# Kernel tuning notes

Hardware: AMD Instinct MI355X
Metric: run time of the kernel (lower is better)

The kernel has to match this reference:

```python
import jax, jax.numpy as jnp
import numpy as np
import math

REG = 0.1      # entropic regularization (self.reg)
TEMP = 0.1     # self.temperature from kwargs
ITERS = 20     # self.iters
EPS = 1e-5     # torch LayerNorm eps
ALPHA_BOTH = -100.0


def _layernorm(t, g, b):
    mu = jnp.mean(t, axis=-1, keepdims=True)
    var = jnp.mean((t - mu) ** 2, axis=-1, keepdims=True)
    return (t - mu) / jnp.sqrt(var + EPS) * g + b


def setup_inputs() -> dict:
    key = jax.random.key(0)
    k1, k2, k3 = jax.random.split(key, 3)
    B, M, N, H = 2048, 36, 36, 768
    x = jax.random.normal(k1, (B, M, H), jnp.float32)
    y = jax.random.normal(k2, (B, N, H), jnp.float32)
    # dustbin scorer params: LayerNorm(H) -> Linear(H, 1)
    ln_g = jnp.ones((H,), jnp.float32)
    ln_b = jnp.zeros((H,), jnp.float32)
    w = jax.random.normal(k3, (H, 1), jnp.float32) * (1.0 / math.sqrt(H))
    b_lin = jnp.zeros((1,), jnp.float32)
    return {"x": x, "y": y, "ln_g": ln_g, "ln_b": ln_b, "w": w, "b_lin": b_lin}


def reference(x, y, ln_g, ln_b, w, b_lin):
    B, M, H = x.shape
    N = y.shape[1]
    # CosineScorer(temperature=1).score(x, y, get_diag=False)
    xn = x / jnp.linalg.norm(x, axis=-1, keepdims=True)
    yn = y / jnp.linalg.norm(y, axis=-1, keepdims=True)
    scores = jnp.einsum('bmh,bnh->bmn', xn, yn)            # (B, M, N)
    # tanh-clipped learned dustbin scores
    ax = jnp.tanh(_layernorm(x, ln_g, ln_b) @ w + b_lin)   # (B, M, 1)
    ay = jnp.tanh(_layernorm(y, ln_g, ln_b) @ w + b_lin)   # (B, N, 1)
    # augmented score matrix with dustbin row/col
    alpha_both = jnp.full((B, 1, 1), ALPHA_BOTH, scores.dtype)
    top = jnp.concatenate([scores, ax], axis=2)                       # (B, M, N+1)
    bot = jnp.concatenate([jnp.swapaxes(ay, 1, 2), alpha_both], axis=2)  # (B, 1, N+1)
    couplings = jnp.concatenate([top, bot], axis=1) / REG             # (B, M+1, N+1)
    # SuperGlue-style marginals: dustbins absorb the complementary mass
    norm_c = -math.log(M + N)
    log_mu = jnp.concatenate([jnp.full((M,), norm_c),
                              jnp.array([math.log(N) + norm_c])]).astype(scores.dtype)
    log_nu = jnp.concatenate([jnp.full((N,), norm_c),
                              jnp.array([math.log(M) + norm_c])]).astype(scores.dtype)

    def body(carry, _):
        u, v = carry
        u = log_mu[None, :] - jax.nn.logsumexp(couplings + v[:, None, :], axis=2)
        v = log_nu[None, :] - jax.nn.logsumexp(couplings + u[:, :, None], axis=1)
        return (u, v), None

    u0 = jnp.zeros((B, M + 1), scores.dtype)
    v0 = jnp.zeros((B, N + 1), scores.dtype)
    (u, v), _ = jax.lax.scan(body, (u0, v0), None, length=ITERS)
    Z = couplings + u[:, :, None] + v[:, None, :] - norm_c            # log matching, (B, M+1, N+1)
    # scalar alignment score per batch element: <P, S> / temperature
    total = jnp.sum(jnp.exp(Z[:, :-1, :-1]) * scores, axis=(1, 2)) / TEMP
    return Z, total
```

## Files before the change

### kernel.cpp

```cpp
#include <hip/hip_runtime.h>
#include <stdint.h>
#include <stddef.h>


typedef float  f4  __attribute__((ext_vector_type(4)));
typedef short  s8v __attribute__((ext_vector_type(8)));
typedef unsigned int u2v __attribute__((ext_vector_type(2)));

#define HD   768
#define MR   36
#define KC   128
#define NCH  6
#define AS   136
#define CS   44
#define LOG2E 1.4426950408889634f
#define LN2   0.6931471805599453f
#define L272  6.169925001442312f
#define KC2   (10.0f*LOG2E)
#define NEGB  (-1.0e30f)

__device__ __forceinline__ uint32_t pkbf2(float a, float b) {
    uint32_t ua = __float_as_uint(a), ub = __float_as_uint(b);
    ua += 0x7FFFu + ((ua >> 16) & 1u);
    ub += 0x7FFFu + ((ub >> 16) & 1u);
    return (ua >> 16) | (ub & 0xFFFF0000u);
}

__global__ __launch_bounds__(256, 3) void sinkhorn_kernel(
    const float* __restrict__ X, const float* __restrict__ Y,
    const float* __restrict__ LG, const float* __restrict__ LB,
    const float* __restrict__ W,  const float* __restrict__ BL,
    float* __restrict__ OUT, int NB)
{
    __shared__ __align__(16) uint16_t Al[48 * AS];
    __shared__ __align__(16) uint16_t Bt[48 * AS];
    __shared__ __align__(16) float C2 [37 * CS];
    __shared__ __align__(16) float C2T[37 * CS];
    __shared__ __align__(16) float u_l[40];
    __shared__ __align__(16) float v_l[40];
    __shared__ float stx[MR * 3], sty[MR * 3];
    __shared__ float rnx[MR], rny[MR];
    __shared__ float s_gw, s_bw, red[4];

    const int t  = threadIdx.x;
    const int b  = blockIdx.x;
    const int wv = t >> 6, ln = t & 63;
    const int c4 = t & 31, gg = t >> 5;

    if (t < 40) { u_l[t] = 0.0f; v_l[t] = 0.0f; }
    if (t < 37) {
        C2 [t * CS + 37] = NEGB; C2 [t * CS + 38] = NEGB; C2 [t * CS + 39] = NEGB;
        C2T[t * CS + 37] = NEGB; C2T[t * CS + 38] = NEGB; C2T[t * CS + 39] = NEGB;
    }
    if (wv == 3) {
        float a = 0.0f, c = 0.0f;
        for (int q = 0; q < 12; ++q) {
            int h = ln + 64 * q;
            float wval = W[h];
            a += LG[h] * wval; c += LB[h] * wval;
        }
        for (int o = 32; o > 0; o >>= 1) { a += __shfl_down(a, o); c += __shfl_down(c, o); }
        if (ln == 0) { s_gw = a; s_bw = c; }
    }

    float sx[5][3], sy[5][3];
    #pragma unroll
    for (int p = 0; p < 5; ++p)
        #pragma unroll
        for (int s = 0; s < 3; ++s) { sx[p][s] = 0.0f; sy[p][s] = 0.0f; }

    f4 acc[3];
    #pragma unroll
    for (int i = 0; i < 3; ++i) acc[i] = (f4){0.0f, 0.0f, 0.0f, 0.0f};

    const float* xb = X + (size_t)b * (MR * HD);
    const float* yb = Y + (size_t)b * (MR * HD);

    const int frow = ln & 15, fq = ln >> 4;
    const int rA = (wv * 16 + frow) * AS + fq * 8;

    for (int kc = 0; kc < NCH; ++kc) {
        const int k0 = kc * KC;
        f4 gv = *(const f4*)(LG + k0 + c4 * 4);
        f4 wvec = *(const f4*)(W + k0 + c4 * 4);
        f4 gw = gv * wvec;
        #pragma unroll
        for (int p = 0; p < 5; ++p) {
            if (p < 4 || t < 128) {
                const int row = (p < 4) ? (p * 8 + gg) : (32 + gg);
                f4 xv = *(const f4*)(xb + row * HD + k0 + c4 * 4);
                sx[p][0] += (xv.x + xv.y) + (xv.z + xv.w);
                sx[p][1] += xv.x * xv.x + xv.y * xv.y + xv.z * xv.z + xv.w * xv.w;
                sx[p][2] += xv.x * gw.x + xv.y * gw.y + xv.z * gw.z + xv.w * gw.w;
                u2v px; px.x = pkbf2(xv.x, xv.y); px.y = pkbf2(xv.z, xv.w);
                *(u2v*)&Al[row * AS + c4 * 4] = px;
                f4 yv = *(const f4*)(yb + row * HD + k0 + c4 * 4);
                sy[p][0] += (yv.x + yv.y) + (yv.z + yv.w);
                sy[p][1] += yv.x * yv.x + yv.y * yv.y + yv.z * yv.z + yv.w * yv.w;
                sy[p][2] += yv.x * gw.x + yv.y * gw.y + yv.z * gw.z + yv.w * gw.w;
                u2v py; py.x = pkbf2(yv.x, yv.y); py.y = pkbf2(yv.z, yv.w);
                *(u2v*)&Bt[row * AS + c4 * 4] = py;
            }
        }
        __syncthreads();
        if (wv < 3) {
            #pragma unroll
            for (int ks = 0; ks < 4; ++ks) {
                s8v af = *(const s8v*)&Al[rA + ks * 32];
                #pragma unroll
                for (int tn = 0; tn < 3; ++tn) {
                    s8v bf = *(const s8v*)&Bt[(tn * 16 + frow) * AS + fq * 8 + ks * 32];
                    acc[tn] = __builtin_amdgcn_mfma_f32_16x16x32_bf16(af, bf, acc[tn], 0, 0, 0);
                }
            }
        }
        __syncthreads();
    }

    #pragma unroll
    for (int p = 0; p < 5; ++p) {
        const int row = (p < 4) ? (p * 8 + gg) : (32 + gg);
        #pragma unroll
        for (int s = 0; s < 3; ++s) {
            float a = sx[p][s], c = sy[p][s];
            for (int o = 16; o > 0; o >>= 1) { a += __shfl_down(a, o, 32); c += __shfl_down(c, o, 32); }
            if ((t & 31) == 0 && row < MR) { stx[row * 3 + s] = a; sty[row * 3 + s] = c; }
        }
    }
    __syncthreads();

    {
        const float blin = BL[0];
        if (t < MR) {
            float Sx = stx[t * 3], Sxx = stx[t * 3 + 1], Sxw = stx[t * 3 + 2];
            rnx[t] = __builtin_amdgcn_rsqf(Sxx);
            float mu  = Sx * (1.0f / HD);
            float var = Sxx * (1.0f / HD) - mu * mu;
            float rsd = __builtin_amdgcn_rsqf(var + 1e-5f);
            float lin = (Sxw - mu * s_gw) * rsd + s_bw + blin;
            float e   = __builtin_amdgcn_exp2f(2.0f * LOG2E * lin);
            float th  = (e - 1.0f) / (e + 1.0f);
            C2 [t * CS + 36] = th * KC2;
            C2T[36 * CS + t] = th * KC2;
        } else if (t >= 64 && t < 64 + MR) {
            int j = t - 64;
            float Sy = sty[j * 3], Syy = sty[j * 3 + 1], Syw = sty[j * 3 + 2];
            rny[j] = __builtin_amdgcn_rsqf(Syy);
            float mu  = Sy * (1.0f / HD);
            float var = Syy * (1.0f / HD) - mu * mu;
            float rsd = __builtin_amdgcn_rsqf(var + 1e-5f);
            float lin = (Syw - mu * s_gw) * rsd + s_bw + blin;
            float e   = __builtin_amdgcn_exp2f(2.0f * LOG2E * lin);
            float th  = (e - 1.0f) / (e + 1.0f);
            C2 [36 * CS + j] = th * KC2;
            C2T[j * CS + 36] = th * KC2;
        } else if (t == 128) {
            C2 [36 * CS + 36] = -100.0f * KC2;
            C2T[36 * CS + 36] = -100.0f * KC2;
        }
    }
    __syncthreads();

    if (wv < 3) {
        #pragma unroll
        for (int tn = 0; tn < 3; ++tn) {
            #pragma unroll
            for (int r = 0; r < 4; ++r) {
                int i = wv * 16 + fq * 4 + r;
                int j = tn * 16 + frow;
                if (i < MR && j < MR) {
                    float v = acc[tn][r] * rnx[i] * rny[j] * KC2;
                    C2 [i * CS + j] = v;
                    C2T[j * CS + i] = v;
                }
            }
        }
    }
    __syncthreads();

    if (wv == 0 && ln < 37) {
        const int i = ln;
        const float lmu = (i < MR) ? -L272 : -1.0f;
        f4 cr[10], ct[10];
        #pragma unroll
        for (int jj = 0; jj < 10; ++jj) {
            cr[jj] = *(const f4*)(&C2 [i * CS + jj * 4]);
            ct[jj] = *(const f4*)(&C2T[i * CS + jj * 4]);
        }
        for (int it = 0; it < 20; ++it) {
            float tt[40];
            float m = -3.0e38f;
            #pragma unroll
            for (int jj = 0; jj < 10; ++jj) {
                f4 vv = *(const f4*)(&v_l[jj * 4]);
                f4 s = cr[jj] + vv;
                tt[jj*4+0] = s.x; tt[jj*4+1] = s.y; tt[jj*4+2] = s.z; tt[jj*4+3] = s.w;
                m = fmaxf(m, fmaxf(fmaxf(s.x, s.y), fmaxf(s.z, s.w)));
            }
            float ss = 0.0f;
            #pragma unroll
            for (int jj = 0; jj < 10; ++jj)
                ss += __builtin_amdgcn_exp2f(tt[jj*4+0] - m) + __builtin_amdgcn_exp2f(tt[jj*4+1] - m)
                    + __builtin_amdgcn_exp2f(tt[jj*4+2] - m) + __builtin_amdgcn_exp2f(tt[jj*4+3] - m);
            u_l[i] = lmu - (m + __builtin_amdgcn_logf(ss));
            m = -3.0e38f;
            #pragma unroll
            for (int jj = 0; jj < 10; ++jj) {
                f4 uu = *(const f4*)(&u_l[jj * 4]);
                f4 s = ct[jj] + uu;
                tt[jj*4+0] = s.x; tt[jj*4+1] = s.y; tt[jj*4+2] = s.z; tt[jj*4+3] = s.w;
                m = fmaxf(m, fmaxf(fmaxf(s.x, s.y), fmaxf(s.z, s.w)));
            }
            ss = 0.0f;
            #pragma unroll
            for (int jj = 0; jj < 10; ++jj)
                ss += __builtin_amdgcn_exp2f(tt[jj*4+0] - m) + __builtin_amdgcn_exp2f(tt[jj*4+1] - m)
                    + __builtin_amdgcn_exp2f(tt[jj*4+2] - m) + __builtin_amdgcn_exp2f(tt[jj*4+3] - m);
            v_l[i] = lmu - (m + __builtin_amdgcn_logf(ss));
        }
    }
    __syncthreads();

    float tot = 0.0f;
    const size_t ob = (size_t)b * 1369;
    for (int e = t; e < 1369; e += 256) {
        int i = e / 37, j = e - i * 37;
        float c2v = C2[i * CS + j];
        float z2  = c2v + u_l[i] + v_l[j] + L272;
        OUT[ob + e] = z2 * LN2;
        if (i < MR && j < MR)
            tot += __builtin_amdgcn_exp2f(z2) * (c2v * (0.1f * LN2));
    }
    for (int o = 32; o > 0; o >>= 1) tot += __shfl_down(tot, o);
    if (ln == 0) red[wv] = tot;
    __syncthreads();
    if (t == 0) OUT[(size_t)NB * 1369 + b] = (red[0] + red[1] + red[2] + red[3]) * 10.0f;
}

extern "C" void kernel_launch(void* const* d_in, const int* in_sizes, int n_in,
                              void* d_out, int out_size, void* d_ws, size_t ws_size,
                              hipStream_t stream) {
    const float* X  = (const float*)d_in[0];
    const float* Y  = (const float*)d_in[1];
    const float* LG = (const float*)d_in[2];
    const float* LB = (const float*)d_in[3];
    const float* W  = (const float*)d_in[4];
    const float* BL = (const float*)d_in[5];
    const int NB = in_sizes[0] / (MR * HD);
    hipLaunchKernelGGL(sinkhorn_kernel, dim3(NB), dim3(256), 0, stream,
                       X, Y, LG, LB, W, BL, (float*)d_out, NB);
}
```

Measured before the change: 519.2 us.

## Split into build and per-wave Sinkhorn kernels with register prefetch of inputs

Splits the fused kernel in two. The first kernel computes the cosine and dustbin score matrix and writes it to workspace. The second runs four batch elements per block, one wavefront each, so the serial 20-iteration Sinkhorn loop no longer leaves three of four waves idle in every block. The build kernel also prefetches the next K-chunk of X and Y into registers while the MFMAs run, and raises the occupancy target. In exchange it adds a global round trip of the score matrix, a second launch, and the column values are now held in registers per thread.

```diff
diff --git a/kernel.cpp b/kernel.cpp
--- a/kernel.cpp
+++ b/kernel.cpp
@@ -12,7 +12,6 @@
 #define KC   128
 #define NCH  6
 #define AS   136
-#define CS   44
 #define LOG2E 1.4426950408889634f
 #define LN2   0.6931471805599453f
 #define L272  6.169925001442312f
@@ -26,32 +25,24 @@
     return (ua >> 16) | (ub & 0xFFFF0000u);
 }
 
-__global__ __launch_bounds__(256, 3) void sinkhorn_kernel(
+__global__ __launch_bounds__(256, 4) void build_kernel(
     const float* __restrict__ X, const float* __restrict__ Y,
     const float* __restrict__ LG, const float* __restrict__ LB,
     const float* __restrict__ W,  const float* __restrict__ BL,
-    float* __restrict__ OUT, int NB)
+    float* __restrict__ C2G, int NB)
 {
     __shared__ __align__(16) uint16_t Al[48 * AS];
     __shared__ __align__(16) uint16_t Bt[48 * AS];
-    __shared__ __align__(16) float C2 [37 * CS];
-    __shared__ __align__(16) float C2T[37 * CS];
-    __shared__ __align__(16) float u_l[40];
-    __shared__ __align__(16) float v_l[40];
+    __shared__ __align__(16) float Cst[37 * 40];
     __shared__ float stx[MR * 3], sty[MR * 3];
     __shared__ float rnx[MR], rny[MR];
-    __shared__ float s_gw, s_bw, red[4];
+    __shared__ float s_gw, s_bw;
 
     const int t  = threadIdx.x;
     const int b  = blockIdx.x;
     const int wv = t >> 6, ln = t & 63;
     const int c4 = t & 31, gg = t >> 5;
 
-    if (t < 40) { u_l[t] = 0.0f; v_l[t] = 0.0f; }
-    if (t < 37) {
-        C2 [t * CS + 37] = NEGB; C2 [t * CS + 38] = NEGB; C2 [t * CS + 39] = NEGB;
-        C2T[t * CS + 37] = NEGB; C2T[t * CS + 38] = NEGB; C2T[t * CS + 39] = NEGB;
-    }
     if (wv == 3) {
         float a = 0.0f, c = 0.0f;
         for (int q = 0; q < 12; ++q) {
@@ -79,22 +70,34 @@
     const int frow = ln & 15, fq = ln >> 4;
     const int rA = (wv * 16 + frow) * AS + fq * 8;
 
-    for (int kc = 0; kc < NCH; ++kc) {
-        const int k0 = kc * KC;
-        f4 gv = *(const f4*)(LG + k0 + c4 * 4);
-        f4 wvec = *(const f4*)(W + k0 + c4 * 4);
-        f4 gw = gv * wvec;
+    f4 xr[5], yr[5];
+    {
+        const int k0 = 0;
         #pragma unroll
         for (int p = 0; p < 5; ++p) {
             if (p < 4 || t < 128) {
                 const int row = (p < 4) ? (p * 8 + gg) : (32 + gg);
-                f4 xv = *(const f4*)(xb + row * HD + k0 + c4 * 4);
+                xr[p] = *(const f4*)(xb + row * HD + k0 + c4 * 4);
+                yr[p] = *(const f4*)(yb + row * HD + k0 + c4 * 4);
+            }
+        }
+    }
+
+    for (int kc = 0; kc < NCH; ++kc) {
+        const int k0 = kc * KC;
+        f4 gv   = *(const f4*)(LG + k0 + c4 * 4);
+        f4 wvec = *(const f4*)(W  + k0 + c4 * 4);
+        f4 gw = gv * wvec;
+        #pragma unroll
+        for (int p = 0; p < 5; ++p) {
+            if (p < 4 || t < 128) {
+                const int row = (p < 4) ? (p * 8 + gg) : (32 + gg);
+                f4 xv = xr[p], yv = yr[p];
                 sx[p][0] += (xv.x + xv.y) + (xv.z + xv.w);
                 sx[p][1] += xv.x * xv.x + xv.y * xv.y + xv.z * xv.z + xv.w * xv.w;
                 sx[p][2] += xv.x * gw.x + xv.y * gw.y + xv.z * gw.z + xv.w * gw.w;
                 u2v px; px.x = pkbf2(xv.x, xv.y); px.y = pkbf2(xv.z, xv.w);
                 *(u2v*)&Al[row * AS + c4 * 4] = px;
-                f4 yv = *(const f4*)(yb + row * HD + k0 + c4 * 4);
                 sy[p][0] += (yv.x + yv.y) + (yv.z + yv.w);
                 sy[p][1] += yv.x * yv.x + yv.y * yv.y + yv.z * yv.z + yv.w * yv.w;
                 sy[p][2] += yv.x * gw.x + yv.y * gw.y + yv.z * gw.z + yv.w * gw.w;
@@ -103,6 +106,17 @@
             }
         }
         __syncthreads();
+        if (kc < NCH - 1) {
+            const int k1 = k0 + KC;
+            #pragma unroll
+            for (int p = 0; p < 5; ++p) {
+                if (p < 4 || t < 128) {
+                    const int row = (p < 4) ? (p * 8 + gg) : (32 + gg);
+                    xr[p] = *(const f4*)(xb + row * HD + k1 + c4 * 4);
+                    yr[p] = *(const f4*)(yb + row * HD + k1 + c4 * 4);
+                }
+            }
+        }
         if (wv < 3) {
             #pragma unroll
             for (int ks = 0; ks < 4; ++ks) {
@@ -140,8 +154,7 @@
             float lin = (Sxw - mu * s_gw) * rsd + s_bw + blin;
             float e   = __builtin_amdgcn_exp2f(2.0f * LOG2E * lin);
             float th  = (e - 1.0f) / (e + 1.0f);
-            C2 [t * CS + 36] = th * KC2;
-            C2T[36 * CS + t] = th * KC2;
+            Cst[t * 40 + 36] = th * KC2;
         } else if (t >= 64 && t < 64 + MR) {
             int j = t - 64;
             float Sy = sty[j * 3], Syy = sty[j * 3 + 1], Syw = sty[j * 3 + 2];
@@ -152,11 +165,13 @@
             float lin = (Syw - mu * s_gw) * rsd + s_bw + blin;
             float e   = __builtin_amdgcn_exp2f(2.0f * LOG2E * lin);
             float th  = (e - 1.0f) / (e + 1.0f);
-            C2 [36 * CS + j] = th * KC2;
-            C2T[j * CS + 36] = th * KC2;
+            Cst[36 * 40 + j] = th * KC2;
         } else if (t == 128) {
-            C2 [36 * CS + 36] = -100.0f * KC2;
-            C2T[36 * CS + 36] = -100.0f * KC2;
+            Cst[36 * 40 + 36] = -100.0f * KC2;
+        }
+        if (t >= 160 && t < 160 + 37) {
+            int i = t - 160;
+            Cst[i * 40 + 37] = NEGB; Cst[i * 40 + 38] = NEGB; Cst[i * 40 + 39] = NEGB;
         }
     }
     __syncthreads();
@@ -168,73 +183,92 @@
             for (int r = 0; r < 4; ++r) {
                 int i = wv * 16 + fq * 4 + r;
                 int j = tn * 16 + frow;
-                if (i < MR && j < MR) {
-                    float v = acc[tn][r] * rnx[i] * rny[j] * KC2;
-                    C2 [i * CS + j] = v;
-                    C2T[j * CS + i] = v;
-                }
+                if (i < MR && j < MR)
+                    Cst[i * 40 + j] = acc[tn][r] * rnx[i] * rny[j] * KC2;
             }
         }
     }
     __syncthreads();
 
-    if (wv == 0 && ln < 37) {
-        const int i = ln;
-        const float lmu = (i < MR) ? -L272 : -1.0f;
-        f4 cr[10], ct[10];
+    {
+        f4* dst = (f4*)(C2G + (size_t)b * 1480);
+        const f4* src = (const f4*)Cst;
+        for (int q = t; q < 370; q += 256) dst[q] = src[q];
+    }
+}
+
+__global__ __launch_bounds__(256, 2) void sink_kernel(
+    const float* __restrict__ C2G, float* __restrict__ OUT, int NB)
+{
+    __shared__ __align__(16) float Cl[4][1480];
+    __shared__ __align__(16) float ub[4][40];
+    __shared__ __align__(16) float vb[4][40];
+
+    const int t = threadIdx.x, wv = t >> 6, ln = t & 63;
+    const int b = blockIdx.x * 4 + wv;
+    if (b >= NB) return;
+
+    float* Cw = &Cl[wv][0];
+    {
+        const f4* src = (const f4*)(C2G + (size_t)b * 1480);
+        f4* dst = (f4*)Cw;
+        for (int q = ln; q < 370; q += 64) dst[q] = src[q];
+    }
+    if (ln < 40) { ub[wv][ln] = 0.0f; vb[wv][ln] = 0.0f; }
+
+    const int r = (ln < 37) ? ln : 36;
+    f4 cr[10];
+    float ct[40];
+    #pragma unroll
+    for (int jj = 0; jj < 10; ++jj) cr[jj] = *(const f4*)&Cw[r * 40 + jj * 4];
+    #pragma unroll
+    for (int j = 0; j < 37; ++j) ct[j] = Cw[j * 40 + r];
+    ct[37] = NEGB; ct[38] = NEGB; ct[39] = NEGB;
+
+    const float lmu = (ln < 36) ? -L272 : -1.0f;
+
+    for (int it = 0; it < 20; ++it) {
+        float tt[40];
+        float m = -3.0e38f;
         #pragma unroll
         for (int jj = 0; jj < 10; ++jj) {
-            cr[jj] = *(const f4*)(&C2 [i * CS + jj * 4]);
-            ct[jj] = *(const f4*)(&C2T[i * CS + jj * 4]);
-        }
-        for (int it = 0; it < 20; ++it) {
-            float tt[40];
-            float m = -3.0e38f;
-            #pragma unroll
-            for (int jj = 0; jj < 10; ++jj) {
-                f4 vv = *(const f4*)(&v_l[jj * 4]);
-                f4 s = cr[jj] + vv;
-                tt[jj*4+0] = s.x; tt[jj*4+1] = s.y; tt[jj*4+2] = s.z; tt[jj*4+3] = s.w;
-                m = fmaxf(m, fmaxf(fmaxf(s.x, s.y), fmaxf(s.z, s.w)));
-            }
-            float ss = 0.0f;
-            #pragma unroll
-            for (int jj = 0; jj < 10; ++jj)
-                ss += __builtin_amdgcn_exp2f(tt[jj*4+0] - m) + __builtin_amdgcn_exp2f(tt[jj*4+1] - m)
-                    + __builtin_amdgcn_exp2f(tt[jj*4+2] - m) + __builtin_amdgcn_exp2f(tt[jj*4+3] - m);
-            u_l[i] = lmu - (m + __builtin_amdgcn_logf(ss));
-            m = -3.0e38f;
-            #pragma unroll
-            for (int jj = 0; jj < 10; ++jj) {
-                f4 uu = *(const f4*)(&u_l[jj * 4]);
-                f4 s = ct[jj] + uu;
-                tt[jj*4+0] = s.x; tt[jj*4+1] = s.y; tt[jj*4+2] = s.z; tt[jj*4+3] = s.w;
-                m = fmaxf(m, fmaxf(fmaxf(s.x, s.y), fmaxf(s.z, s.w)));
-            }
-            ss = 0.0f;
-            #pragma unroll
-            for (int jj = 0; jj < 10; ++jj)
-                ss += __builtin_amdgcn_exp2f(tt[jj*4+0] - m) + __builtin_amdgcn_exp2f(tt[jj*4+1] - m)
-                    + __builtin_amdgcn_exp2f(tt[jj*4+2] - m) + __builtin_amdgcn_exp2f(tt[jj*4+3] - m);
-            v_l[i] = lmu - (m + __builtin_amdgcn_logf(ss));
-        }
-    }
-    __syncthreads();
+            f4 vv = *(const f4*)&vb[wv][jj * 4];
+            f4 s = cr[jj] + vv;
+            tt[jj*4+0] = s.x; tt[jj*4+1] = s.y; tt[jj*4+2] = s.z; tt[jj*4+3] = s.w;
+            m = fmaxf(m, fmaxf(fmaxf(s.x, s.y), fmaxf(s.z, s.w)));
+        }
+        float ss = 0.0f;
+        #pragma unroll
+        for (int k = 0; k < 40; ++k) ss += __builtin_amdgcn_exp2f(tt[k] - m);
+        if (ln < 37) ub[wv][ln] = lmu - (m + __builtin_amdgcn_logf(ss));
+
+        m = -3.0e38f;
+        #pragma unroll
+        for (int jj = 0; jj < 10; ++jj) {
+            f4 uu = *(const f4*)&ub[wv][jj * 4];
+            f4 cv = *(const f4*)&ct[jj * 4];
+            f4 s = cv + uu;
+            tt[jj*4+0] = s.x; tt[jj*4+1] = s.y; tt[jj*4+2] = s.z; tt[jj*4+3] = s.w;
+            m = fmaxf(m, fmaxf(fmaxf(s.x, s.y), fmaxf(s.z, s.w)));
+        }
+        ss = 0.0f;
+        #pragma unroll
+        for (int k = 0; k < 40; ++k) ss += __builtin_amdgcn_exp2f(tt[k] - m);
+        if (ln < 37) vb[wv][ln] = lmu - (m + __builtin_amdgcn_logf(ss));
+    }
 
     float tot = 0.0f;
     const size_t ob = (size_t)b * 1369;
-    for (int e = t; e < 1369; e += 256) {
+    for (int e = ln; e < 1369; e += 64) {
         int i = e / 37, j = e - i * 37;
-        float c2v = C2[i * CS + j];
-        float z2  = c2v + u_l[i] + v_l[j] + L272;
+        float c2v = Cw[i * 40 + j];
+        float z2  = c2v + ub[wv][i] + vb[wv][j] + L272;
         OUT[ob + e] = z2 * LN2;
         if (i < MR && j < MR)
             tot += __builtin_amdgcn_exp2f(z2) * (c2v * (0.1f * LN2));
     }
     for (int o = 32; o > 0; o >>= 1) tot += __shfl_down(tot, o);
-    if (ln == 0) red[wv] = tot;
-    __syncthreads();
-    if (t == 0) OUT[(size_t)NB * 1369 + b] = (red[0] + red[1] + red[2] + red[3]) * 10.0f;
+    if (ln == 0) OUT[(size_t)NB * 1369 + b] = tot * 10.0f;
 }
 
 extern "C" void kernel_launch(void* const* d_in, const int* in_sizes, int n_in,
@@ -247,6 +281,9 @@
     const float* W  = (const float*)d_in[4];
     const float* BL = (const float*)d_in[5];
     const int NB = in_sizes[0] / (MR * HD);
-    hipLaunchKernelGGL(sinkhorn_kernel, dim3(NB), dim3(256), 0, stream,
-                       X, Y, LG, LB, W, BL, (float*)d_out, NB);
-}
+    float* C2G = (float*)d_ws;
+    hipLaunchKernelGGL(build_kernel, dim3(NB), dim3(256), 0, stream,
+                       X, Y, LG, LB, W, BL, C2G, NB);
+    hipLaunchKernelGGL(sink_kernel, dim3((NB + 3) / 4), dim3(256), 0, stream,
+                       C2G, (float*)d_out, NB);
+}
```

After: 541.6 us. 1.04x slower.
